# Optimization experiments

Measured on AMD Instinct MI355X. Metric: run time of the kernel, lower is better.

## Reference

```python
import jax, jax.numpy as jnp
import numpy as np

DIM = 64
HEADS = 4            # self.num_heads = 2 * num_heads(=2)
SMK = 5
KS = 7
EPS = 1e-5
SCALE = (DIM // HEADS) ** -0.5


def pool_mat(n, out=7):
    # AdaptiveAvgPool2d bin matrix: P[i, j] = 1/size if floor(i*n/out) <= j < ceil((i+1)*n/out)
    P = np.zeros((out, n), np.float32)
    for i in range(out):
        s = (i * n) // out
        e = -((-(i + 1) * n) // out)
        P[i, s:e] = 1.0 / (e - s)
    return jnp.asarray(P)


def bn(x, g, b, m, v):
    # inference BatchNorm2d on [B,C,H,W]
    return (x - m[:, None, None]) * (g[:, None, None] * jax.lax.rsqrt(v[:, None, None] + EPS)) + b[:, None, None]


def conv1x1(x, w):
    return jnp.einsum('oi,bihw->bohw', w, x)


def rpb_bias(rpb, H, W, k):
    # replicate apply_rpb gather indexing (incl. the flip over flattened HW)
    rs = 2 * k - 1
    ih0 = np.arange(k)
    idx_k = (ih0[:, None] * rs + ih0[None, :]).reshape(-1)        # [k*k]
    rh = np.ones(k, np.int64); rh[k // 2] = H - (k - 1)
    rw = np.ones(k, np.int64); rw[k // 2] = W - (k - 1)
    ih = np.repeat(ih0, rh)                                       # [H]
    iw = np.repeat(ih0, rw)                                       # [W]
    bias_hw = ih[:, None] * rs + iw[None, :]                      # [H,W]
    bias_idx = (bias_hw[..., None] + idx_k).reshape(-1, k * k)[::-1].copy()  # [H*W,k*k]
    flat = rpb.reshape(rpb.shape[0], -1)                          # [G, rs*rs]
    return flat[:, bias_idx].reshape(1, rpb.shape[0], H, W, k * k)


def na2d_av(attn, value, k):
    # NATTEN-style neighborhood AV: window start clamped to stay in-bounds
    B, G, H, W, _ = attn.shape
    si = np.clip(np.arange(H) - k // 2, 0, H - k)
    sj = np.clip(np.arange(W) - k // 2, 0, W - k)
    ii = si[:, None] + np.arange(k)    # [H,k]
    jj = sj[:, None] + np.arange(k)    # [W,k]
    v = value[:, :, ii][:, :, :, :, jj]         # [B,G,H,k,W,k,C]
    a = attn.reshape(B, G, H, W, k, k)
    return jnp.einsum('bghwij,bghiwjc->bghwc', a, v)


def reference(x, wq_w, wq_g, wq_b, wq_m, wq_v,
              wk_w, wk_g, wk_b, wk_m, wk_v,
              proj_w, proj_b, rpb1, rpb2,
              dy_w, dy_g, dy_b, dy_m, dy_v):
    B, C, H, W = x.shape
    G = HEADS
    q, kctx = jnp.split(x, 2, axis=1)                      # [B,C/2,H,W] each
    q = bn(conv1x1(q, wq_w), wq_g, wq_b, wq_m, wq_v) * SCALE
    Ph, Pw = pool_mat(H), pool_mat(W)
    kp = jnp.einsum('ph,bchw,qw->bcpq', Ph, kctx, Pw)      # adaptive avg pool to 7x7
    k = bn(conv1x1(kp, wk_w), wk_g, wk_b, wk_m, wk_v)
    q = q.reshape(B, G, -1, H * W)                          # b g c n
    k = k.reshape(B, G, -1, 49)                             # b g c l
    w = jnp.einsum('bgcn,bgcl->bgnl', q, k)
    w = w.transpose(0, 3, 1, 2)                             # b l g n
    w = jnp.einsum('ol,blgn->bogn', proj_w, w) + proj_b[None, :, None, None]  # b (74) g n
    w = w.transpose(0, 2, 3, 1).reshape(B, G, H, W, SMK * SMK + KS * KS)
    attn1 = w[..., :SMK * SMK]
    attn2 = w[..., SMK * SMK:]
    attn1 = jax.nn.softmax(attn1 + rpb_bias(rpb1, H, W, SMK), axis=-1)
    attn2 = jax.nn.softmax(attn2 + rpb_bias(rpb2, H, W, KS), axis=-1)
    c = C // (2 * G)
    value = x.reshape(B, 2, G, c, H, W).transpose(1, 0, 2, 4, 5, 3)  # m b g h w c
    x1 = na2d_av(attn1, value[0], SMK)
    x2 = na2d_av(attn2, value[1], KS)
    out = jnp.concatenate([x1, x2], axis=1)                 # b (2g) h w c
    out = out.transpose(0, 1, 4, 2, 3).reshape(B, C, H, W)  # b (g c) h w
    return bn(conv1x1(out, dy_w), dy_g, dy_b, dy_m, dy_v)


def setup_inputs() -> dict:
    key = jax.random.key(0)
    ks = jax.random.split(key, 20)
    h = DIM // 2
    def bnp(k):
        k1, k2, k3, k4 = jax.random.split(k, 4)
        return (jax.random.uniform(k1, (0,)),)  # unused
    inp = {
        'x': jax.random.normal(ks[0], (8, DIM, 64, 64), jnp.float32),
        'wq_w': jax.random.normal(ks[1], (h, h), jnp.float32) * (h ** -0.5),
        'wq_g': jax.random.uniform(ks[2], (h,), jnp.float32, 0.5, 1.5),
        'wq_b': jax.random.normal(ks[3], (h,), jnp.float32) * 0.1,
        'wq_m': jax.random.normal(ks[4], (h,), jnp.float32) * 0.1,
        'wq_v': jax.random.uniform(ks[5], (h,), jnp.float32, 0.5, 1.5),
        'wk_w': jax.random.normal(ks[6], (h, h), jnp.float32) * (h ** -0.5),
        'wk_g': jax.random.uniform(ks[7], (h,), jnp.float32, 0.5, 1.5),
        'wk_b': jax.random.normal(ks[8], (h,), jnp.float32) * 0.1,
        'wk_m': jax.random.normal(ks[9], (h,), jnp.float32) * 0.1,
        'wk_v': jax.random.uniform(ks[10], (h,), jnp.float32, 0.5, 1.5),
        'proj_w': jax.random.normal(ks[11], (SMK * SMK + KS * KS, 49), jnp.float32) * (49 ** -0.5),
        'proj_b': jax.random.normal(ks[12], (SMK * SMK + KS * KS,), jnp.float32) * 0.02,
        'rpb1': jax.random.normal(ks[13], (HEADS, 2 * SMK - 1, 2 * SMK - 1), jnp.float32) * 0.02,
        'rpb2': jax.random.normal(ks[14], (HEADS, 2 * KS - 1, 2 * KS - 1), jnp.float32) * 0.02,
        'dy_w': jax.random.normal(ks[15], (DIM, DIM), jnp.float32) * (DIM ** -0.5),
        'dy_g': jax.random.uniform(ks[16], (DIM,), jnp.float32, 0.5, 1.5),
        'dy_b': jax.random.normal(ks[17], (DIM,), jnp.float32) * 0.1,
        'dy_m': jax.random.normal(ks[18], (DIM,), jnp.float32) * 0.1,
        'dy_v': jax.random.uniform(ks[19], (DIM,), jnp.float32, 0.5, 1.5),
    }
    return inp
```

## Files before the change

kernel.cpp:

```cpp
#include <hip/hip_runtime.h>

#define EPSV 1e-5f

#define OFF_W    12544
#define OFF_WQ2  31488
#define OFF_Q0   32512
#define OFF_DYT  32544

typedef float f4u __attribute__((ext_vector_type(4), aligned(4)));

__global__ __launch_bounds__(256) void pool_prep_kernel(
    const float* __restrict__ x,
    const float* __restrict__ wk_w, const float* __restrict__ wk_g,
    const float* __restrict__ wk_b, const float* __restrict__ wk_m,
    const float* __restrict__ wk_v,
    const float* __restrict__ wq_w, const float* __restrict__ wq_g,
    const float* __restrict__ wq_b, const float* __restrict__ wq_m,
    const float* __restrict__ wq_v,
    const float* __restrict__ dy_w,
    float* __restrict__ ws)
{
  __shared__ float s_tmp[32 * 64];
  __shared__ float s_kp[32 * 7];
  const int tid = threadIdx.x;

  if (blockIdx.x >= 56) {
    const int t = (blockIdx.x - 56) * 256 + tid;
    for (int idx = t; idx < 1056; idx += 2048) {
      if (idx < 1024) {
        const int i = idx >> 5, o = idx & 31;
        const float s = wq_g[o] * rsqrtf(wq_v[o] + EPSV);
        ws[OFF_WQ2 + idx] = 0.25f * s * wq_w[o * 32 + i];
      } else {
        const int o = idx - 1024;
        const float s = wq_g[o] * rsqrtf(wq_v[o] + EPSV);
        ws[OFF_Q0 + o] = 0.25f * (wq_b[o] - wq_m[o] * s);
      }
    }
    for (int idx = t; idx < 4096; idx += 2048) {
      const int i = idx >> 6, o = idx & 63;
      ws[OFF_DYT + idx] = dy_w[o * 64 + i];
    }
    return;
  }

  const int b = blockIdx.x / 7;
  const int p = blockIdx.x % 7;
  const int sh = (p * 64) / 7, eh = ((p + 1) * 64 + 6) / 7;
  const float invH = 1.0f / (float)(eh - sh);
  for (int idx = tid; idx < 2048; idx += 256) {
    const int c = idx >> 6, ww = idx & 63;
    const float* xp = x + ((size_t)(b * 64 + 32 + c)) * 4096 + ww;
    float s = 0.f;
    for (int hh = sh; hh < eh; ++hh) s += xp[hh * 64];
    s_tmp[idx] = s * invH;
  }
  __syncthreads();
  if (tid < 224) {
    const int c = tid / 7, q = tid % 7;
    const int sw = (q * 64) / 7, ew = ((q + 1) * 64 + 6) / 7;
    float s = 0.f;
    for (int ww = sw; ww < ew; ++ww) s += s_tmp[c * 64 + ww];
    s_kp[c * 7 + q] = s / (float)(ew - sw);
  }
  __syncthreads();
  if (tid < 224) {
    const int o = tid / 7, q = tid % 7;
    float s = 0.f;
#pragma unroll
    for (int i = 0; i < 32; i++) s += wk_w[o * 32 + i] * s_kp[i * 7 + q];
    const float sc = wk_g[o] * rsqrtf(wk_v[o] + EPSV);
    const int g = o >> 3, c = o & 7, l = p * 7 + q;
    ws[(((size_t)b * 4 + g) * 8 + c) * 49 + l] = (s - wk_m[o]) * sc + wk_b[o];
  }
}

__global__ __launch_bounds__(256) void fold_w_kernel(
    const float* __restrict__ proj_w, const float* __restrict__ ws_in,
    float* __restrict__ Wout)
{
  const int bg = blockIdx.x;
  const int tid = threadIdx.x;
  __shared__ float s_k[392];
  for (int i = tid; i < 392; i += 256) s_k[i] = ws_in[(size_t)bg * 392 + i];
  __syncthreads();
  for (int idx = tid; idx < 592; idx += 256) {
    const int o = idx >> 3, c = idx & 7;
    float s = 0.f;
#pragma unroll
    for (int l = 0; l < 49; l++) s += proj_w[o * 49 + l] * s_k[c * 49 + l];
    Wout[(size_t)bg * 592 + idx] = s;
  }
}

template <int K, int R0, int R1, int PBASE>
__device__ __forceinline__ void attn_part(
    const float* __restrict__ Wr, const float* __restrict__ proj_b,
    const float* __restrict__ rp, const float* __restrict__ vb,
    int si, int sj, const float* q8, float* acc, float& den)
{
  constexpr int RS = 2 * K - 1;
  constexpr int NP = (R1 - R0) * K;
  float l[NP];
#pragma unroll
  for (int i = R0; i < R1; i++)
#pragma unroll
    for (int j = 0; j < K; j++) {
      const int p = i * K + j;
      const float* wo = Wr + (PBASE + p) * 8;
      float s = proj_b[PBASE + p];
#pragma unroll
      for (int c = 0; c < 8; c++) s += wo[c] * q8[c];
      l[(i - R0) * K + j] = s + rp[i * RS + j];
    }
  float p0 = 0.f, p1 = 0.f, p2 = 0.f, p3 = 0.f;
#pragma unroll
  for (int o = 0; o < NP; o++) {
    const float e = __expf(l[o]);
    l[o] = e;
    if ((o & 3) == 0) p0 += e;
    else if ((o & 3) == 1) p1 += e;
    else if ((o & 3) == 2) p2 += e;
    else p3 += e;
  }
  den = (p0 + p1) + (p2 + p3);
#pragma unroll
  for (int c = 0; c < 8; c++) acc[c] = 0.f;
#pragma unroll
  for (int i = R0; i < R1; i++) {
    const float* vr0 = vb + (si + i) * 64 + sj;
#pragma unroll
    for (int c = 0; c < 8; c++) {
      const float* vr = vr0 + c * 4096;
      if constexpr (K == 5) {
        const f4u f = *(const f4u*)vr;
        const float v4 = vr[4];
        acc[c] += l[(i - R0) * 5 + 0] * f.x + l[(i - R0) * 5 + 1] * f.y +
                  l[(i - R0) * 5 + 2] * f.z + l[(i - R0) * 5 + 3] * f.w +
                  l[(i - R0) * 5 + 4] * v4;
      } else {
        const f4u fa = *(const f4u*)vr;
        const f4u fb = *(const f4u*)(vr + 3);
        acc[c] += l[(i - R0) * 7 + 0] * fa.x + l[(i - R0) * 7 + 1] * fa.y +
                  l[(i - R0) * 7 + 2] * fa.z + l[(i - R0) * 7 + 3] * fa.w +
                  l[(i - R0) * 7 + 4] * fb.y + l[(i - R0) * 7 + 5] * fb.z +
                  l[(i - R0) * 7 + 6] * fb.w;
      }
    }
  }
}

__global__ __launch_bounds__(1024, 4) void contmix_main(
    const float* __restrict__ x,
    const float* __restrict__ proj_b,
    const float* __restrict__ rpb1, const float* __restrict__ rpb2,
    const float* __restrict__ dy_g, const float* __restrict__ dy_b,
    const float* __restrict__ dy_m, const float* __restrict__ dy_v,
    const float* __restrict__ ws,
    float* __restrict__ out)
{
  __shared__ float s_val[64 * 64];
  __shared__ float s_den[512];
  __shared__ float s_rpb1[324];
  __shared__ float s_rpb2[676];

  const int b = blockIdx.x >> 6;
  const int h = blockIdx.x & 63;
  const int tid = threadIdx.x;
  const int w = tid & 63;
  const int gu  = __builtin_amdgcn_readfirstlane((tid >> 6) & 3);
  const int bru = __builtin_amdgcn_readfirstlane((tid >> 8) & 1);
  const int hfu = __builtin_amdgcn_readfirstlane(tid >> 9);

  for (int i = tid; i < 324; i += 1024) s_rpb1[i] = rpb1[i];
  for (int i = tid; i < 676; i += 1024) s_rpb2[i] = rpb2[i];
  __syncthreads();

  const float* xb = x + (size_t)b * 64 * 4096;

  float q8[8];
  {
    const float* q0 = ws + OFF_Q0 + gu * 8;
#pragma unroll
    for (int o = 0; o < 8; o++) q8[o] = q0[o];
    const float* wq2 = ws + OFF_WQ2 + gu * 8;
#pragma unroll
    for (int i = 0; i < 32; i++) {
      const float xv = xb[i * 4096 + h * 64 + w];
#pragma unroll
      for (int o = 0; o < 8; o++) q8[o] += wq2[i * 32 + o] * xv;
    }
  }

  const float* Wr = ws + OFF_W + (size_t)(b * 4 + gu) * 592;
  const int ph = 63 - h, pw = 63 - w;

  float acc[8];
  float den;
  if (bru == 0) {
    const int bih = ph - min(max(ph - 2, 0), 59);
    const int biw = pw - min(max(pw - 2, 0), 59);
    const int si = min(max(h - 2, 0), 59), sj = min(max(w - 2, 0), 59);
    const float* rp = s_rpb1 + gu * 81 + bih * 9 + biw;
    const float* vb = xb + gu * 8 * 4096;
    if (hfu == 0)
      attn_part<5, 0, 3, 0>(Wr, proj_b, rp, vb, si, sj, q8, acc, den);
    else
      attn_part<5, 3, 5, 0>(Wr, proj_b, rp, vb, si, sj, q8, acc, den);
  } else {
    const int bih = ph - min(max(ph - 3, 0), 57);
    const int biw = pw - min(max(pw - 3, 0), 57);
    const int si = min(max(h - 3, 0), 57), sj = min(max(w - 3, 0), 57);
    const float* rp = s_rpb2 + gu * 169 + bih * 13 + biw;
    const float* vb = xb + (32 + gu * 8) * 4096;
    if (hfu == 0)
      attn_part<7, 0, 4, 25>(Wr, proj_b, rp, vb, si, sj, q8, acc, den);
    else
      attn_part<7, 4, 7, 25>(Wr, proj_b, rp, vb, si, sj, q8, acc, den);
  }

  const int chbase = bru * 32 + gu * 8;
  if (hfu == 0) {
    s_den[(bru * 4 + gu) * 64 + w] = den;
#pragma unroll
    for (int c = 0; c < 8; c++) s_val[(chbase + c) * 64 + w] = acc[c];
  }
  __syncthreads();
  if (hfu == 1) {
    const float inv = 1.f / (s_den[(bru * 4 + gu) * 64 + w] + den);
#pragma unroll
    for (int c = 0; c < 8; c++)
      s_val[(chbase + c) * 64 + w] =
          (s_val[(chbase + c) * 64 + w] + acc[c]) * inv;
  }
  __syncthreads();

  {
    const int og = __builtin_amdgcn_readfirstlane(tid >> 6);
    float facc[4];
#pragma unroll
    for (int oo = 0; oo < 4; oo++) facc[oo] = 0.f;
    const float* dyt = ws + OFF_DYT + og * 4;
#pragma unroll
    for (int i = 0; i < 64; i++) {
      const float v = s_val[i * 64 + w];
#pragma unroll
      for (int oo = 0; oo < 4; oo++) facc[oo] += dyt[i * 64 + oo] * v;
    }
#pragma unroll
    for (int oo = 0; oo < 4; oo++) {
      const int oc = og * 4 + oo;
      const float sc = dy_g[oc] * rsqrtf(dy_v[oc] + EPSV);
      out[((size_t)(b * 64 + oc)) * 4096 + h * 64 + w] =
          (facc[oo] - dy_m[oc]) * sc + dy_b[oc];
    }
  }
}

extern "C" void kernel_launch(void* const* d_in, const int* in_sizes, int n_in,
                              void* d_out, int out_size, void* d_ws, size_t ws_size,
                              hipStream_t stream)
{
  const float* x      = (const float*)d_in[0];
  const float* wq_w   = (const float*)d_in[1];
  const float* wq_g   = (const float*)d_in[2];
  const float* wq_b   = (const float*)d_in[3];
  const float* wq_m   = (const float*)d_in[4];
  const float* wq_v   = (const float*)d_in[5];
  const float* wk_w   = (const float*)d_in[6];
  const float* wk_g   = (const float*)d_in[7];
  const float* wk_b   = (const float*)d_in[8];
  const float* wk_m   = (const float*)d_in[9];
  const float* wk_v   = (const float*)d_in[10];
  const float* proj_w = (const float*)d_in[11];
  const float* proj_b = (const float*)d_in[12];
  const float* rpb1   = (const float*)d_in[13];
  const float* rpb2   = (const float*)d_in[14];
  const float* dy_w   = (const float*)d_in[15];
  const float* dy_g   = (const float*)d_in[16];
  const float* dy_b   = (const float*)d_in[17];
  const float* dy_m   = (const float*)d_in[18];
  const float* dy_v   = (const float*)d_in[19];

  float* ws = (float*)d_ws;

  pool_prep_kernel<<<64, 256, 0, stream>>>(x, wk_w, wk_g, wk_b, wk_m, wk_v,
                                           wq_w, wq_g, wq_b, wq_m, wq_v,
                                           dy_w, ws);
  fold_w_kernel<<<32, 256, 0, stream>>>(proj_w, ws, ws + OFF_W);
  contmix_main<<<512, 1024, 0, stream>>>(x, proj_b, rpb1, rpb2,
                                         dy_g, dy_b, dy_m, dy_v,
                                         ws, (float*)d_out);
}
```

Measured before the change: 173.3 us.

## Share query projection across warps via LDS and stream softmax per row

Each block now stages its row of the query half of x into shared memory and computes the 32 projected query channels once, two per warp, instead of every thread recomputing its 8-channel group from global loads. The weight layout is transposed so each warp reads contiguous rows. The attention part now computes logits, exponentials and the denominator one window row at a time rather than holding all logits in registers. Together these cut register pressure so launch bounds can ask for 8 waves per SIMD, at the cost of extra LDS and a second barrier.

```diff
diff --git a/kernel.cpp b/kernel.cpp
--- a/kernel.cpp
+++ b/kernel.cpp
@@ -28,9 +28,9 @@
     const int t = (blockIdx.x - 56) * 256 + tid;
     for (int idx = t; idx < 1056; idx += 2048) {
       if (idx < 1024) {
-        const int i = idx >> 5, o = idx & 31;
+        const int o = idx >> 5;
         const float s = wq_g[o] * rsqrtf(wq_v[o] + EPSV);
-        ws[OFF_WQ2 + idx] = 0.25f * s * wq_w[o * 32 + i];
+        ws[OFF_WQ2 + idx] = 0.25f * s * wq_w[idx];
       } else {
         const int o = idx - 1024;
         const float s = wq_g[o] * rsqrtf(wq_v[o] + EPSV);
@@ -100,34 +100,22 @@
     int si, int sj, const float* q8, float* acc, float& den)
 {
   constexpr int RS = 2 * K - 1;
-  constexpr int NP = (R1 - R0) * K;
-  float l[NP];
-#pragma unroll
-  for (int i = R0; i < R1; i++)
+  den = 0.f;
+#pragma unroll
+  for (int c = 0; c < 8; c++) acc[c] = 0.f;
+#pragma unroll
+  for (int i = R0; i < R1; i++) {
+    float l[K];
 #pragma unroll
     for (int j = 0; j < K; j++) {
-      const int p = i * K + j;
-      const float* wo = Wr + (PBASE + p) * 8;
-      float s = proj_b[PBASE + p];
+      const int p = PBASE + i * K + j;
+      const float* wo = Wr + p * 8;
+      float s = proj_b[p];
 #pragma unroll
       for (int c = 0; c < 8; c++) s += wo[c] * q8[c];
-      l[(i - R0) * K + j] = s + rp[i * RS + j];
-    }
-  float p0 = 0.f, p1 = 0.f, p2 = 0.f, p3 = 0.f;
-#pragma unroll
-  for (int o = 0; o < NP; o++) {
-    const float e = __expf(l[o]);
-    l[o] = e;
-    if ((o & 3) == 0) p0 += e;
-    else if ((o & 3) == 1) p1 += e;
-    else if ((o & 3) == 2) p2 += e;
-    else p3 += e;
-  }
-  den = (p0 + p1) + (p2 + p3);
-#pragma unroll
-  for (int c = 0; c < 8; c++) acc[c] = 0.f;
-#pragma unroll
-  for (int i = R0; i < R1; i++) {
+      l[j] = __expf(s + rp[i * RS + j]);
+      den += l[j];
+    }
     const float* vr0 = vb + (si + i) * 64 + sj;
 #pragma unroll
     for (int c = 0; c < 8; c++) {
@@ -135,22 +123,18 @@
       if constexpr (K == 5) {
         const f4u f = *(const f4u*)vr;
         const float v4 = vr[4];
-        acc[c] += l[(i - R0) * 5 + 0] * f.x + l[(i - R0) * 5 + 1] * f.y +
-                  l[(i - R0) * 5 + 2] * f.z + l[(i - R0) * 5 + 3] * f.w +
-                  l[(i - R0) * 5 + 4] * v4;
+        acc[c] += l[0] * f.x + l[1] * f.y + l[2] * f.z + l[3] * f.w + l[4] * v4;
       } else {
         const f4u fa = *(const f4u*)vr;
         const f4u fb = *(const f4u*)(vr + 3);
-        acc[c] += l[(i - R0) * 7 + 0] * fa.x + l[(i - R0) * 7 + 1] * fa.y +
-                  l[(i - R0) * 7 + 2] * fa.z + l[(i - R0) * 7 + 3] * fa.w +
-                  l[(i - R0) * 7 + 4] * fb.y + l[(i - R0) * 7 + 5] * fb.z +
-                  l[(i - R0) * 7 + 6] * fb.w;
+        acc[c] += l[0] * fa.x + l[1] * fa.y + l[2] * fa.z + l[3] * fa.w +
+                  l[4] * fb.y + l[5] * fb.z + l[6] * fb.w;
       }
     }
   }
 }
 
-__global__ __launch_bounds__(1024, 4) void contmix_main(
+__global__ __launch_bounds__(1024, 8) void contmix_main(
     const float* __restrict__ x,
     const float* __restrict__ proj_b,
     const float* __restrict__ rpb1, const float* __restrict__ rpb2,
@@ -160,6 +144,8 @@
     float* __restrict__ out)
 {
   __shared__ float s_val[64 * 64];
+  __shared__ float s_xa[32 * 64];
+  __shared__ float s_q[32 * 64];
   __shared__ float s_den[512];
   __shared__ float s_rpb1[324];
   __shared__ float s_rpb2[676];
@@ -172,25 +158,38 @@
   const int bru = __builtin_amdgcn_readfirstlane((tid >> 8) & 1);
   const int hfu = __builtin_amdgcn_readfirstlane(tid >> 9);
 
+  const float* xb = x + (size_t)b * 64 * 4096;
+
+  {
+    const float* xr = xb + h * 64;
+#pragma unroll
+    for (int idx = tid; idx < 2048; idx += 1024)
+      s_xa[idx] = xr[(size_t)(idx >> 6) * 4096 + (idx & 63)];
+  }
   for (int i = tid; i < 324; i += 1024) s_rpb1[i] = rpb1[i];
   for (int i = tid; i < 676; i += 1024) s_rpb2[i] = rpb2[i];
   __syncthreads();
 
-  const float* xb = x + (size_t)b * 64 * 4096;
+  {
+    const int oc0 = __builtin_amdgcn_readfirstlane((tid >> 6) * 2);
+    const float* wr0 = ws + OFF_WQ2 + oc0 * 32;
+    const float* wr1 = wr0 + 32;
+    float a0 = ws[OFF_Q0 + oc0];
+    float a1 = ws[OFF_Q0 + oc0 + 1];
+#pragma unroll
+    for (int i = 0; i < 32; i++) {
+      const float xv = s_xa[i * 64 + w];
+      a0 += wr0[i] * xv;
+      a1 += wr1[i] * xv;
+    }
+    s_q[oc0 * 64 + w] = a0;
+    s_q[(oc0 + 1) * 64 + w] = a1;
+  }
+  __syncthreads();
 
   float q8[8];
-  {
-    const float* q0 = ws + OFF_Q0 + gu * 8;
-#pragma unroll
-    for (int o = 0; o < 8; o++) q8[o] = q0[o];
-    const float* wq2 = ws + OFF_WQ2 + gu * 8;
-#pragma unroll
-    for (int i = 0; i < 32; i++) {
-      const float xv = xb[i * 4096 + h * 64 + w];
-#pragma unroll
-      for (int o = 0; o < 8; o++) q8[o] += wq2[i * 32 + o] * xv;
-    }
-  }
+#pragma unroll
+  for (int c = 0; c < 8; c++) q8[c] = s_q[(gu * 8 + c) * 64 + w];
 
   const float* Wr = ws + OFF_W + (size_t)(b * 4 + gu) * 592;
   const int ph = 63 - h, pw = 63 - w;
```

New measurement: 167.0 us. 1.04x faster.
